# Kernel tuning notes

Measured on AMD Instinct MI355X. Metric: run time of the kernel, lower is better.

Reference implementation:

```python
import jax, jax.numpy as jnp
import numpy as np

B, NW, H, K = 64, 256, 768, 4
K1, Bp, AVDL = 0.1, 1.2, 50.0
ALPHA = 1.0 / H  # 1 / interaction_rep_size
BETA = 0.1


def setup_inputs() -> dict:
    key = jax.random.key(0)
    k1, k2, k3, k4, k5, k6 = jax.random.split(key, 6)
    return {
        "q_rep": jax.random.normal(k1, (B, NW, H), dtype=jnp.float32),
        "d_rep": jax.random.normal(k2, (B, NW, H), dtype=jnp.float32),
        "qtw": jax.random.uniform(k3, (B, NW), dtype=jnp.float32),
        "q_input_ids": jax.random.randint(k4, (B, NW, K), 0, 32, dtype=jnp.int32),
        "d_input_ids": jax.random.randint(k5, (B, NW, K), 0, 32, dtype=jnp.int32),
        "d_tfs": jax.random.randint(k6, (B, NW), 0, 10, dtype=jnp.int32),
    }


def _null_mask(input_ids):
    # [B, NW, 1] float mask: 0 where the whole window is zero ids
    all_zero = jnp.all(input_ids == 0, axis=2)
    return (~all_zero).astype(jnp.float32)[:, :, None]


def reference(q_rep, d_rep, qtw, q_input_ids, d_input_ids, d_tfs):
    q = q_rep * _null_mask(q_input_ids)
    d = d_rep * _null_mask(d_input_ids)

    # term-overlap scores: [B, NW, NW]
    d_expanded_tf = jnp.einsum("bqh,bdh->bqd", q, d)

    # exact match between q windows and d windows: [B, NW, NW]
    em_f = jnp.all(q_input_ids[:, :, None, :] == d_input_ids[:, None, :, :],
                   axis=3).astype(jnp.float32)

    # blended expanded term frequency, weighted by doc term frequencies
    d_tf = d_expanded_tf * (ALPHA * BETA) + em_f * (1.0 - BETA)
    tf_mult = d_tfs.astype(jnp.float32)[:, None, :]          # [B, 1, NW]
    expanded_term_df = jnp.sum(d_tf * tf_mult, axis=2)       # [B, NW]

    # BM25-like scoring
    dl = jnp.sum(d_tfs.astype(jnp.float32), axis=1, keepdims=True)  # [B, 1]
    denom = expanded_term_df * (1.0 + K1)
    nom = expanded_term_df + K1 * (1.0 - Bp + Bp * dl / AVDL)
    dtw = denom / (nom + 1e-8)
    s = jnp.sum(qtw * dtw, axis=1)                           # [B]
    return s, d_expanded_tf
```

## Files before the change

### kernel.cpp

```cpp
#include <hip/hip_runtime.h>
#include <hip/hip_bf16.h>

#define B_   64
#define NW_  256
#define H_   768

#define AB_    (0.1f / 768.0f)
#define OMB_   0.9f
#define K1_    0.1f
#define BP_    1.2f
#define AVDL_  50.0f

typedef __bf16 bf16x4 __attribute__((ext_vector_type(4)));
typedef __bf16 bf16x8 __attribute__((ext_vector_type(8)));
typedef float  f32x4  __attribute__((ext_vector_type(4)));

#define BAR_LGKM() asm volatile("s_waitcnt lgkmcnt(0)\n\ts_barrier" ::: "memory")

__global__ __launch_bounds__(256, 1) void gemm_fused(
    const float* __restrict__ q_rep, const float* __restrict__ d_rep,
    const int* __restrict__ q_ids, const int* __restrict__ d_ids,
    const int* __restrict__ d_tfs,
    float* __restrict__ S, float* __restrict__ ws_etdf)
{
    __shared__ __align__(16) __bf16 As[2][128][40];
    __shared__ __align__(16) __bf16 Bs[2][128][40];
    __shared__ float mq_s[128];
    __shared__ float md_s[128];
    __shared__ float mdtf_s[128];
    __shared__ float tf_s[128];
    __shared__ int4  qk_s[128];
    __shared__ int4  dk_s[128];

    const int tid  = threadIdx.x;
    const int wave = tid >> 6;
    const int lane = tid & 63;
    const int bid  = blockIdx.x;
    const int b    = bid & 63;
    const int t    = bid >> 6;
    const int m0   = (t & 1) * 128;
    const int n0   = (t >> 1) * 128;

    if (tid < 128) {
        int4 qa = *(const int4*)(q_ids + ((size_t)b * NW_ + m0 + tid) * 4);
        qk_s[tid] = qa;
        mq_s[tid] = (qa.x == 0 && qa.y == 0 && qa.z == 0 && qa.w == 0) ? 0.f : 1.f;
    } else {
        const int r = tid - 128;
        int4 da = *(const int4*)(d_ids + ((size_t)b * NW_ + n0 + r) * 4);
        dk_s[r] = da;
        float md = (da.x == 0 && da.y == 0 && da.z == 0 && da.w == 0) ? 0.f : 1.f;
        float tf = (float)d_tfs[(size_t)b * NW_ + n0 + r];
        md_s[r]   = md;
        tf_s[r]   = tf;
        mdtf_s[r] = md * tf;
    }

    const int srow = tid >> 3;
    const int sseg = tid & 7;
    const float* Abase = q_rep + ((size_t)b * NW_ + m0) * H_;
    const float* Bbase = d_rep + ((size_t)b * NW_ + n0) * H_;

    float4 ra0[4], rb0[4], ra1[4], rb1[4], ra2[4], rb2[4];

    auto loadg = [&](float4 (&ra)[4], float4 (&rb)[4], int kc) {
#pragma unroll
        for (int i = 0; i < 4; ++i) {
            const int row = i * 32 + srow;
            ra[i] = *(const float4*)(Abase + (size_t)row * H_ + kc * 32 + sseg * 4);
            rb[i] = *(const float4*)(Bbase + (size_t)row * H_ + kc * 32 + sseg * 4);
        }
    };
    auto stage = [&](float4 (&ra)[4], float4 (&rb)[4], int buf) {
#pragma unroll
        for (int i = 0; i < 4; ++i) {
            const int row = i * 32 + srow;
            bf16x4 va = { (__bf16)ra[i].x, (__bf16)ra[i].y,
                          (__bf16)ra[i].z, (__bf16)ra[i].w };
            *(bf16x4*)&As[buf][row][sseg * 4] = va;
            bf16x4 vb = { (__bf16)rb[i].x, (__bf16)rb[i].y,
                          (__bf16)rb[i].z, (__bf16)rb[i].w };
            *(bf16x4*)&Bs[buf][row][sseg * 4] = vb;
        }
    };

    f32x4 acc[4][4];
#pragma unroll
    for (int i = 0; i < 4; ++i)
#pragma unroll
        for (int j = 0; j < 4; ++j)
            acc[i][j] = (f32x4){0.f, 0.f, 0.f, 0.f};

    const int fr = lane & 15;
    const int fk = (lane >> 4) * 8;
    const int qm = wave >> 1;
    const int qn = wave & 1;

    loadg(ra0, rb0, 0);
    loadg(ra1, rb1, 1);
    loadg(ra2, rb2, 2);
    stage(ra0, rb0, 0);
    BAR_LGKM();

#pragma unroll
    for (int kc = 0; kc < 24; ++kc) {
        const int buf = kc & 1;
        if (kc < 21) {
            if (kc % 3 == 0)      loadg(ra0, rb0, kc + 3);
            else if (kc % 3 == 1) loadg(ra1, rb1, kc + 3);
            else                  loadg(ra2, rb2, kc + 3);
        }
        bf16x8 af[4], bfr[4];
#pragma unroll
        for (int t4 = 0; t4 < 4; ++t4) {
            af[t4]  = *(bf16x8*)&As[buf][qm * 64 + t4 * 16 + fr][fk];
            bfr[t4] = *(bf16x8*)&Bs[buf][qn * 64 + t4 * 16 + fr][fk];
        }
#pragma unroll
        for (int i = 0; i < 4; ++i)
#pragma unroll
            for (int j = 0; j < 4; ++j)
                acc[i][j] = __builtin_amdgcn_mfma_f32_16x16x32_bf16(
                    af[i], bfr[j], acc[i][j], 0, 0, 0);
        if (kc < 23) {
            const int nb = buf ^ 1;
            if ((kc + 1) % 3 == 0)      stage(ra0, rb0, nb);
            else if ((kc + 1) % 3 == 1) stage(ra1, rb1, nb);
            else                        stage(ra2, rb2, nb);
        }
        BAR_LGKM();
    }

    const int cn = lane & 15;
    const int qg = lane >> 4;
    float md_l[4], mdtf_l[4], tf_l[4];
    int4  dk_l[4];
#pragma unroll
    for (int j = 0; j < 4; ++j) {
        const int c = qn * 64 + j * 16 + cn;
        md_l[j]   = md_s[c];
        mdtf_l[j] = mdtf_s[c];
        tf_l[j]   = tf_s[c];
        dk_l[j]   = dk_s[c];
    }
    float* Sbase = S + ((size_t)b * NW_ + m0 + qm * 64) * NW_ + n0 + qn * 64;

    float rs[16];
#pragma unroll
    for (int i = 0; i < 4; ++i)
#pragma unroll
        for (int r = 0; r < 4; ++r) {
            const int row = i * 16 + qg * 4 + r;
            const float mq = mq_s[qm * 64 + row];
            const int4  qk = qk_s[qm * 64 + row];
            float sdot = 0.f, sem = 0.f;
#pragma unroll
            for (int j = 0; j < 4; ++j) {
                const float v = acc[i][j][r];
                Sbase[(size_t)row * NW_ + j * 16 + cn] = v * mq * md_l[j];
                sdot += v * mdtf_l[j];
                const int4 dk = dk_l[j];
                if (dk.x == qk.x && dk.y == qk.y && dk.z == qk.z && dk.w == qk.w)
                    sem += tf_l[j];
            }
            rs[i * 4 + r] = mq * AB_ * sdot + OMB_ * sem;
        }
#pragma unroll
    for (int off = 1; off <= 8; off <<= 1)
#pragma unroll
        for (int e = 0; e < 16; ++e)
            rs[e] += __shfl_xor(rs[e], off);
    if (cn == 0) {
#pragma unroll
        for (int i = 0; i < 4; ++i)
#pragma unroll
            for (int r = 0; r < 4; ++r)
                atomicAdd(&ws_etdf[(size_t)b * NW_ + m0 + qm * 64 + i * 16 + qg * 4 + r],
                          rs[i * 4 + r]);
    }
}

__global__ __launch_bounds__(64) void final_kernel(
    const float* __restrict__ ws_etdf, const int* __restrict__ d_tfs,
    const float* __restrict__ qtw, float* __restrict__ out)
{
    const int b = blockIdx.x;
    const int lane = threadIdx.x;

    float4 ev = *(const float4*)(ws_etdf + (size_t)b * NW_ + lane * 4);
    int4  tf4 = *(const int4*)(d_tfs   + (size_t)b * NW_ + lane * 4);
    float4 qv = *(const float4*)(qtw    + (size_t)b * NW_ + lane * 4);

    float dl = (float)(tf4.x + tf4.y + tf4.z + tf4.w);
#pragma unroll
    for (int off = 32; off; off >>= 1) dl += __shfl_xor(dl, off);

    const float c = K1_ * (1.f - BP_ + BP_ * dl / AVDL_);
    float ew[4] = {ev.x, ev.y, ev.z, ev.w};
    float qw[4] = {qv.x, qv.y, qv.z, qv.w};
    float s = 0.f;
#pragma unroll
    for (int j = 0; j < 4; ++j)
        s += qw[j] * (ew[j] * (1.f + K1_)) / (ew[j] + c + 1e-8f);
#pragma unroll
    for (int off = 32; off; off >>= 1) s += __shfl_xor(s, off);
    if (lane == 0) out[b] = s;
}

extern "C" void kernel_launch(void* const* d_in, const int* in_sizes, int n_in,
                              void* d_out, int out_size, void* d_ws, size_t ws_size,
                              hipStream_t stream)
{
    const float* q_rep = (const float*)d_in[0];
    const float* d_rep = (const float*)d_in[1];
    const float* qtw   = (const float*)d_in[2];
    const int*   q_ids = (const int*)d_in[3];
    const int*   d_ids = (const int*)d_in[4];
    const int*   d_tfs = (const int*)d_in[5];

    float* out = (float*)d_out;
    float* S   = out + B_;
    float* ws_etdf = (float*)d_ws;

    hipMemsetAsync(ws_etdf, 0, (size_t)B_ * NW_ * sizeof(float), stream);

    gemm_fused<<<256, 256, 0, stream>>>(q_rep, d_rep, q_ids, d_ids, d_tfs,
                                        S, ws_etdf);
    final_kernel<<<B_, 64, 0, stream>>>(ws_etdf, d_tfs, qtw, out);
}
```

Baseline: 146.0 us.

## Halve the N tile and use 512 threads per block to raise occupancy

The output tile per block shrinks from 128x128 to 128x64, which doubles the grid to 512 blocks. Each block now runs 8 waves of 512 threads, and each wave computes a 32x32 sub-tile instead of 64x64. The aim is to put more waves on each CU to hide global-load latency, since the old grid gave only one 4-wave block per CU. In exchange, each q_rep tile is read four times instead of twice, and the tighter launch bounds cap registers per thread, which may cause spills.

```diff
diff --git a/kernel.cpp b/kernel.cpp
--- a/kernel.cpp
+++ b/kernel.cpp
@@ -17,20 +17,20 @@
 
 #define BAR_LGKM() asm volatile("s_waitcnt lgkmcnt(0)\n\ts_barrier" ::: "memory")
 
-__global__ __launch_bounds__(256, 1) void gemm_fused(
+__global__ __launch_bounds__(512, 4) void gemm_fused(
     const float* __restrict__ q_rep, const float* __restrict__ d_rep,
     const int* __restrict__ q_ids, const int* __restrict__ d_ids,
     const int* __restrict__ d_tfs,
     float* __restrict__ S, float* __restrict__ ws_etdf)
 {
     __shared__ __align__(16) __bf16 As[2][128][40];
-    __shared__ __align__(16) __bf16 Bs[2][128][40];
+    __shared__ __align__(16) __bf16 Bs[2][64][40];
     __shared__ float mq_s[128];
-    __shared__ float md_s[128];
-    __shared__ float mdtf_s[128];
-    __shared__ float tf_s[128];
+    __shared__ float md_s[64];
+    __shared__ float mdtf_s[64];
+    __shared__ float tf_s[64];
     __shared__ int4  qk_s[128];
-    __shared__ int4  dk_s[128];
+    __shared__ int4  dk_s[64];
 
     const int tid  = threadIdx.x;
     const int wave = tid >> 6;
@@ -39,13 +39,13 @@
     const int b    = bid & 63;
     const int t    = bid >> 6;
     const int m0   = (t & 1) * 128;
-    const int n0   = (t >> 1) * 128;
+    const int n0   = (t >> 1) * 64;
 
     if (tid < 128) {
         int4 qa = *(const int4*)(q_ids + ((size_t)b * NW_ + m0 + tid) * 4);
         qk_s[tid] = qa;
         mq_s[tid] = (qa.x == 0 && qa.y == 0 && qa.z == 0 && qa.w == 0) ? 0.f : 1.f;
-    } else {
+    } else if (tid < 192) {
         const int r = tid - 128;
         int4 da = *(const int4*)(d_ids + ((size_t)b * NW_ + n0 + r) * 4);
         dk_s[r] = da;
@@ -61,34 +61,32 @@
     const float* Abase = q_rep + ((size_t)b * NW_ + m0) * H_;
     const float* Bbase = d_rep + ((size_t)b * NW_ + n0) * H_;
 
-    float4 ra0[4], rb0[4], ra1[4], rb1[4], ra2[4], rb2[4];
-
-    auto loadg = [&](float4 (&ra)[4], float4 (&rb)[4], int kc) {
-#pragma unroll
-        for (int i = 0; i < 4; ++i) {
-            const int row = i * 32 + srow;
-            ra[i] = *(const float4*)(Abase + (size_t)row * H_ + kc * 32 + sseg * 4);
-            rb[i] = *(const float4*)(Bbase + (size_t)row * H_ + kc * 32 + sseg * 4);
-        }
+    float4 ra0[2], ra1[2], ra2[2];
+    float4 rb0, rb1, rb2;
+
+    auto loadg = [&](float4 (&ra)[2], float4 &rb, int kc) {
+#pragma unroll
+        for (int i = 0; i < 2; ++i)
+            ra[i] = *(const float4*)(Abase + (size_t)(i * 64 + srow) * H_
+                                     + kc * 32 + sseg * 4);
+        rb = *(const float4*)(Bbase + (size_t)srow * H_ + kc * 32 + sseg * 4);
     };
-    auto stage = [&](float4 (&ra)[4], float4 (&rb)[4], int buf) {
-#pragma unroll
-        for (int i = 0; i < 4; ++i) {
-            const int row = i * 32 + srow;
+    auto stage = [&](float4 (&ra)[2], float4 &rb, int buf) {
+#pragma unroll
+        for (int i = 0; i < 2; ++i) {
             bf16x4 va = { (__bf16)ra[i].x, (__bf16)ra[i].y,
                           (__bf16)ra[i].z, (__bf16)ra[i].w };
-            *(bf16x4*)&As[buf][row][sseg * 4] = va;
-            bf16x4 vb = { (__bf16)rb[i].x, (__bf16)rb[i].y,
-                          (__bf16)rb[i].z, (__bf16)rb[i].w };
-            *(bf16x4*)&Bs[buf][row][sseg * 4] = vb;
-        }
+            *(bf16x4*)&As[buf][i * 64 + srow][sseg * 4] = va;
+        }
+        bf16x4 vb = { (__bf16)rb.x, (__bf16)rb.y, (__bf16)rb.z, (__bf16)rb.w };
+        *(bf16x4*)&Bs[buf][srow][sseg * 4] = vb;
     };
 
-    f32x4 acc[4][4];
-#pragma unroll
-    for (int i = 0; i < 4; ++i)
-#pragma unroll
-        for (int j = 0; j < 4; ++j)
+    f32x4 acc[2][2];
+#pragma unroll
+    for (int i = 0; i < 2; ++i)
+#pragma unroll
+        for (int j = 0; j < 2; ++j)
             acc[i][j] = (f32x4){0.f, 0.f, 0.f, 0.f};
 
     const int fr = lane & 15;
@@ -110,16 +108,16 @@
             else if (kc % 3 == 1) loadg(ra1, rb1, kc + 3);
             else                  loadg(ra2, rb2, kc + 3);
         }
-        bf16x8 af[4], bfr[4];
-#pragma unroll
-        for (int t4 = 0; t4 < 4; ++t4) {
-            af[t4]  = *(bf16x8*)&As[buf][qm * 64 + t4 * 16 + fr][fk];
-            bfr[t4] = *(bf16x8*)&Bs[buf][qn * 64 + t4 * 16 + fr][fk];
-        }
-#pragma unroll
-        for (int i = 0; i < 4; ++i)
-#pragma unroll
-            for (int j = 0; j < 4; ++j)
+        bf16x8 af[2], bfr[2];
+#pragma unroll
+        for (int t2 = 0; t2 < 2; ++t2) {
+            af[t2]  = *(bf16x8*)&As[buf][qm * 32 + t2 * 16 + fr][fk];
+            bfr[t2] = *(bf16x8*)&Bs[buf][qn * 32 + t2 * 16 + fr][fk];
+        }
+#pragma unroll
+        for (int i = 0; i < 2; ++i)
+#pragma unroll
+            for (int j = 0; j < 2; ++j)
                 acc[i][j] = __builtin_amdgcn_mfma_f32_16x16x32_bf16(
                     af[i], bfr[j], acc[i][j], 0, 0, 0);
         if (kc < 23) {
@@ -133,29 +131,29 @@
 
     const int cn = lane & 15;
     const int qg = lane >> 4;
-    float md_l[4], mdtf_l[4], tf_l[4];
-    int4  dk_l[4];
-#pragma unroll
-    for (int j = 0; j < 4; ++j) {
-        const int c = qn * 64 + j * 16 + cn;
+    float md_l[2], mdtf_l[2], tf_l[2];
+    int4  dk_l[2];
+#pragma unroll
+    for (int j = 0; j < 2; ++j) {
+        const int c = qn * 32 + j * 16 + cn;
         md_l[j]   = md_s[c];
         mdtf_l[j] = mdtf_s[c];
         tf_l[j]   = tf_s[c];
         dk_l[j]   = dk_s[c];
     }
-    float* Sbase = S + ((size_t)b * NW_ + m0 + qm * 64) * NW_ + n0 + qn * 64;
-
-    float rs[16];
-#pragma unroll
-    for (int i = 0; i < 4; ++i)
+    float* Sbase = S + ((size_t)b * NW_ + m0 + qm * 32) * NW_ + n0 + qn * 32;
+
+    float rs[8];
+#pragma unroll
+    for (int i = 0; i < 2; ++i)
 #pragma unroll
         for (int r = 0; r < 4; ++r) {
             const int row = i * 16 + qg * 4 + r;
-            const float mq = mq_s[qm * 64 + row];
-            const int4  qk = qk_s[qm * 64 + row];
+            const float mq = mq_s[qm * 32 + row];
+            const int4  qk = qk_s[qm * 32 + row];
             float sdot = 0.f, sem = 0.f;
 #pragma unroll
-            for (int j = 0; j < 4; ++j) {
+            for (int j = 0; j < 2; ++j) {
                 const float v = acc[i][j][r];
                 Sbase[(size_t)row * NW_ + j * 16 + cn] = v * mq * md_l[j];
                 sdot += v * mdtf_l[j];
@@ -168,14 +166,14 @@
 #pragma unroll
     for (int off = 1; off <= 8; off <<= 1)
 #pragma unroll
-        for (int e = 0; e < 16; ++e)
+        for (int e = 0; e < 8; ++e)
             rs[e] += __shfl_xor(rs[e], off);
     if (cn == 0) {
 #pragma unroll
-        for (int i = 0; i < 4; ++i)
+        for (int i = 0; i < 2; ++i)
 #pragma unroll
             for (int r = 0; r < 4; ++r)
-                atomicAdd(&ws_etdf[(size_t)b * NW_ + m0 + qm * 64 + i * 16 + qg * 4 + r],
+                atomicAdd(&ws_etdf[(size_t)b * NW_ + m0 + qm * 32 + i * 16 + qg * 4 + r],
                           rs[i * 4 + r]);
     }
 }
@@ -224,7 +222,7 @@
 
     hipMemsetAsync(ws_etdf, 0, (size_t)B_ * NW_ * sizeof(float), stream);
 
-    gemm_fused<<<256, 256, 0, stream>>>(q_rep, d_rep, q_ids, d_ids, d_tfs,
+    gemm_fused<<<512, 512, 0, stream>>>(q_rep, d_rep, q_ids, d_ids, d_tfs,
                                         S, ws_etdf);
     final_kernel<<<B_, 64, 0, stream>>>(ws_etdf, d_tfs, qtw, out);
 }
```

New measurement: 147.4 us. About the same (+1.0%).

## Stage fp32 tiles directly into LDS via global_load_lds with XOR swizzle

Applied to the files above, without the earlier changes.

Replaces the register-staged global loads plus bf16 conversion stores with direct global-to-LDS 16-byte loads of fp32 data into a double-buffered, XOR-swizzled LDS tile. The fp32-to-bf16 conversion moves to fragment-read time. The aim is to cut VGPR pressure from the three-deep register prefetch and to drop the LDS store instructions. In exchange, LDS holds fp32 (twice the bytes per tile), each thread converts the same data again every time it reads a fragment, and the prefetch depth shrinks from three chunks ahead to one. The explicit minimum-occupancy launch bound is also relaxed.

```diff
diff --git a/kernel.cpp b/kernel.cpp
--- a/kernel.cpp
+++ b/kernel.cpp
@@ -11,20 +11,21 @@
 #define BP_    1.2f
 #define AVDL_  50.0f
 
-typedef __bf16 bf16x4 __attribute__((ext_vector_type(4)));
 typedef __bf16 bf16x8 __attribute__((ext_vector_type(8)));
 typedef float  f32x4  __attribute__((ext_vector_type(4)));
 
-#define BAR_LGKM() asm volatile("s_waitcnt lgkmcnt(0)\n\ts_barrier" ::: "memory")
-
-__global__ __launch_bounds__(256, 1) void gemm_fused(
+#define GLL16(g, l)                                                        \
+    __builtin_amdgcn_global_load_lds(                                      \
+        (const __attribute__((address_space(1))) void*)(g),                \
+        (__attribute__((address_space(3))) void*)(l), 16, 0, 0)
+
+__global__ __launch_bounds__(256) void gemm_fused(
     const float* __restrict__ q_rep, const float* __restrict__ d_rep,
     const int* __restrict__ q_ids, const int* __restrict__ d_ids,
     const int* __restrict__ d_tfs,
     float* __restrict__ S, float* __restrict__ ws_etdf)
 {
-    __shared__ __align__(16) __bf16 As[2][128][40];
-    __shared__ __align__(16) __bf16 Bs[2][128][40];
+    __shared__ __align__(16) float Ls[2][2][128][32];
     __shared__ float mq_s[128];
     __shared__ float md_s[128];
     __shared__ float mdtf_s[128];
@@ -56,33 +57,22 @@
         mdtf_s[r] = md * tf;
     }
 
-    const int srow = tid >> 3;
-    const int sseg = tid & 7;
+    const int srow8 = lane >> 3;
+    const int gseg  = (lane & 7) ^ srow8;
     const float* Abase = q_rep + ((size_t)b * NW_ + m0) * H_;
     const float* Bbase = d_rep + ((size_t)b * NW_ + n0) * H_;
 
-    float4 ra0[4], rb0[4], ra1[4], rb1[4], ra2[4], rb2[4];
-
-    auto loadg = [&](float4 (&ra)[4], float4 (&rb)[4], int kc) {
+    auto stage = [&](int buf, int kc) {
 #pragma unroll
         for (int i = 0; i < 4; ++i) {
-            const int row = i * 32 + srow;
-            ra[i] = *(const float4*)(Abase + (size_t)row * H_ + kc * 32 + sseg * 4);
-            rb[i] = *(const float4*)(Bbase + (size_t)row * H_ + kc * 32 + sseg * 4);
+            const int rbase = i * 32 + wave * 8;
+            const int row   = rbase + srow8;
+            GLL16(Abase + (size_t)row * H_ + kc * 32 + gseg * 4,
+                  &Ls[buf][0][rbase][0]);
+            GLL16(Bbase + (size_t)row * H_ + kc * 32 + gseg * 4,
+                  &Ls[buf][1][rbase][0]);
         }
     };
-    auto stage = [&](float4 (&ra)[4], float4 (&rb)[4], int buf) {
-#pragma unroll
-        for (int i = 0; i < 4; ++i) {
-            const int row = i * 32 + srow;
-            bf16x4 va = { (__bf16)ra[i].x, (__bf16)ra[i].y,
-                          (__bf16)ra[i].z, (__bf16)ra[i].w };
-            *(bf16x4*)&As[buf][row][sseg * 4] = va;
-            bf16x4 vb = { (__bf16)rb[i].x, (__bf16)rb[i].y,
-                          (__bf16)rb[i].z, (__bf16)rb[i].w };
-            *(bf16x4*)&Bs[buf][row][sseg * 4] = vb;
-        }
-    };
 
     f32x4 acc[4][4];
 #pragma unroll
@@ -91,44 +81,41 @@
         for (int j = 0; j < 4; ++j)
             acc[i][j] = (f32x4){0.f, 0.f, 0.f, 0.f};
 
-    const int fr = lane & 15;
-    const int fk = (lane >> 4) * 8;
-    const int qm = wave >> 1;
-    const int qn = wave & 1;
-
-    loadg(ra0, rb0, 0);
-    loadg(ra1, rb1, 1);
-    loadg(ra2, rb2, 2);
-    stage(ra0, rb0, 0);
-    BAR_LGKM();
+    const int fr  = lane & 15;
+    const int fj0 = (lane >> 4) * 2;
+    const int qm  = wave >> 1;
+    const int qn  = wave & 1;
+
+    auto rdfrag = [&](int buf, int mat, int R) -> bf16x8 {
+        const char* rowp = (const char*)&Ls[buf][mat][R][0];
+        const int c = R & 7;
+        float4 v0 = *(const float4*)(rowp + ((fj0 ^ c) * 16));
+        float4 v1 = *(const float4*)(rowp + (((fj0 + 1) ^ c) * 16));
+        return (bf16x8){ (__bf16)v0.x, (__bf16)v0.y, (__bf16)v0.z, (__bf16)v0.w,
+                         (__bf16)v1.x, (__bf16)v1.y, (__bf16)v1.z, (__bf16)v1.w };
+    };
+
+    stage(0, 0);
+    __syncthreads();
 
 #pragma unroll
     for (int kc = 0; kc < 24; ++kc) {
         const int buf = kc & 1;
-        if (kc < 21) {
-            if (kc % 3 == 0)      loadg(ra0, rb0, kc + 3);
-            else if (kc % 3 == 1) loadg(ra1, rb1, kc + 3);
-            else                  loadg(ra2, rb2, kc + 3);
-        }
+        if (kc < 23) stage(buf ^ 1, kc + 1);
         bf16x8 af[4], bfr[4];
 #pragma unroll
-        for (int t4 = 0; t4 < 4; ++t4) {
-            af[t4]  = *(bf16x8*)&As[buf][qm * 64 + t4 * 16 + fr][fk];
-            bfr[t4] = *(bf16x8*)&Bs[buf][qn * 64 + t4 * 16 + fr][fk];
-        }
+        for (int i = 0; i < 4; ++i)
+            af[i] = rdfrag(buf, 0, qm * 64 + i * 16 + fr);
+#pragma unroll
+        for (int j = 0; j < 4; ++j)
+            bfr[j] = rdfrag(buf, 1, qn * 64 + j * 16 + fr);
 #pragma unroll
         for (int i = 0; i < 4; ++i)
 #pragma unroll
             for (int j = 0; j < 4; ++j)
                 acc[i][j] = __builtin_amdgcn_mfma_f32_16x16x32_bf16(
                     af[i], bfr[j], acc[i][j], 0, 0, 0);
-        if (kc < 23) {
-            const int nb = buf ^ 1;
-            if ((kc + 1) % 3 == 0)      stage(ra0, rb0, nb);
-            else if ((kc + 1) % 3 == 1) stage(ra1, rb1, nb);
-            else                        stage(ra2, rb2, nb);
-        }
-        BAR_LGKM();
+        __syncthreads();
     }
 
     const int cn = lane & 15;
```

Result: slower. 160.0 us (+9.6%).
